# Performance work log

Measured on AMD Instinct MI355X. Metric: run time of the kernel, lower is better.

The kernel has to match this reference:

```python
import jax, jax.numpy as jnp
import numpy as np

N, IN, OUT, E, S = 65536, 512, 512, 8, 64


def setup_inputs() -> dict:
    key = jax.random.key(0)
    k1, k2, k3, k4, k5 = jax.random.split(key, 5)
    bound = float(np.sqrt(1.0 / IN))
    x = jax.random.normal(k1, (N, IN), dtype=jnp.float32)
    expert_coefficients = jax.random.normal(k2, (S, E), dtype=jnp.float32)
    batch_indices = jax.random.randint(k3, (N,), 0, S)
    weights = jax.random.uniform(k4, (E, OUT, IN), dtype=jnp.float32, minval=-bound, maxval=bound)
    bias = jax.random.uniform(k5, (OUT,), dtype=jnp.float32, minval=-bound, maxval=bound)
    return {"x": x, "expert_coefficients": expert_coefficients,
            "batch_indices": batch_indices, "weights": weights, "bias": bias}


def reference(x, expert_coefficients, batch_indices, weights, bias):
    # Original computes mixed_weights[b] = sum_e coeff[b,e] * W[e], then for each
    # system b applies mixed_weights[b] to the atoms with batch_indices == b via a
    # masked scan. Linearity lets us equivalently gather per-atom expert
    # coefficients and contract once, avoiding the O(num_systems * N) waste:
    #   out[n,o] = sum_e coeff[batch_indices[n], e] * sum_i W[e,o,i] * x[n,i]
    coeff_per_atom = expert_coefficients[batch_indices]  # [N, E]
    out = jnp.einsum('ni,eoi,ne->no', x, weights, coeff_per_atom)  # [N, OUT]
    return out + bias
```

## Files before the change

### kernel.cpp

```cpp
#include <hip/hip_runtime.h>
#include <hip/hip_bf16.h>

#define NA   65536
#define DIN  512
#define DOUT 512
#define NE   8
#define NS   64
#define CAP  1280
#define BM   128
#define BN   128
#define BK   32
#define TPS  (CAP / BM)

typedef __attribute__((ext_vector_type(8))) __bf16 bf16x8;
typedef __attribute__((ext_vector_type(4))) float floatx4;

__device__ __forceinline__ void async_load16(const void* g, void* l) {
  __builtin_amdgcn_global_load_lds(
      (__attribute__((address_space(1))) void*)(void*)g,
      (__attribute__((address_space(3))) void*)l,
      16, 0, 0);
}

__global__ void scatter_kernel(const int* __restrict__ bidx,
                               int* __restrict__ counts,
                               int* __restrict__ perm) {
  __shared__ int hist[NS];
  __shared__ int base[NS];
  int t = threadIdx.x;
  if (t < NS) hist[t] = 0;
  __syncthreads();
  int n = blockIdx.x * 256 + t;
  int s = bidx[n];
  int rank = atomicAdd(&hist[s], 1);
  __syncthreads();
  if (t < NS && hist[t] > 0) base[t] = atomicAdd(&counts[t], hist[t]);
  __syncthreads();
  perm[s * CAP + base[s] + rank] = n;
}

__global__ void gather_kernel(const float* __restrict__ x,
                              const int* __restrict__ perm,
                              const int* __restrict__ counts,
                              ushort* __restrict__ xp) {
  int rg = blockIdx.x * 4 + (threadIdx.x >> 6);
  int lane = threadIdx.x & 63;
  int s = rg / CAP;
  int r = rg - s * CAP;
  if (r >= counts[s]) return;
  int pr = perm[rg];
  const float4* src = (const float4*)(x + (size_t)pr * DIN);
  float4 a = src[2 * lane], b = src[2 * lane + 1];
  union { bf16x8 v; uint4 u; } cv;
  cv.v[0] = (__bf16)a.x; cv.v[1] = (__bf16)a.y;
  cv.v[2] = (__bf16)a.z; cv.v[3] = (__bf16)a.w;
  cv.v[4] = (__bf16)b.x; cv.v[5] = (__bf16)b.y;
  cv.v[6] = (__bf16)b.z; cv.v[7] = (__bf16)b.w;
  *(uint4*)(xp + (size_t)rg * DIN + lane * 8) = cv.u;
}

__global__ void mixw_kernel(const float* __restrict__ W,
                            const float* __restrict__ coeff,
                            ushort* __restrict__ mixedW) {
  int t = threadIdx.x;
  int base = blockIdx.x * 2048 + t * 8;
  float w[NE][8];
#pragma unroll
  for (int e = 0; e < NE; e++) {
    const float4* p = (const float4*)(W + e * (DOUT * DIN) + base);
    float4 a = p[0], b = p[1];
    w[e][0] = a.x; w[e][1] = a.y; w[e][2] = a.z; w[e][3] = a.w;
    w[e][4] = b.x; w[e][5] = b.y; w[e][6] = b.z; w[e][7] = b.w;
  }
  int s0 = blockIdx.y * 8;
  for (int si = 0; si < 8; si++) {
    int s = s0 + si;
    float o[8] = {0, 0, 0, 0, 0, 0, 0, 0};
#pragma unroll
    for (int e = 0; e < NE; e++) {
      float c = coeff[s * NE + e];
#pragma unroll
      for (int j = 0; j < 8; j++) o[j] += c * w[e][j];
    }
    union { bf16x8 v; uint4 u; } cv;
#pragma unroll
    for (int j = 0; j < 8; j++) cv.v[j] = (__bf16)o[j];
    *(uint4*)(mixedW + (size_t)s * (DOUT * DIN) + base) = cv.u;
  }
}

__global__ __launch_bounds__(256) void gemm_kernel(
    const ushort* __restrict__ xp, const ushort* __restrict__ mixedW,
    const int* __restrict__ perm, const int* __restrict__ counts,
    const float* __restrict__ bias, float* __restrict__ out) {
  int st = blockIdx.y;
  int s = st / TPS;
  int tt = st - s * TPS;
  int count = counts[s];
  int r0 = tt * BM;
  if (r0 >= count) return;
  int rows = min(BM, count - r0);
  int n0 = blockIdx.x * BN;

  __shared__ __align__(16) ushort Alds[2][BM * BK];
  __shared__ __align__(16) ushort Blds[2][BN * BK];
  __shared__ int prow[BM];

  int tid = threadIdx.x;
  int lane = tid & 63;
  int wave = tid >> 6;

  if (tid < BM) prow[tid] = perm[s * CAP + r0 + min(tid, rows - 1)];

  const ushort* aptr[2];
  const ushort* bptr[2];
  int loff[2];
#pragma unroll
  for (int j = 0; j < 2; j++) {
    int region = j * 4 + wave;
    int row = region * 16 + (lane >> 2);
    int kc = (lane & 3) * 8;
    aptr[j] = xp + (size_t)(s * CAP + r0 + row) * DIN + kc;
    bptr[j] = mixedW + (size_t)s * (DOUT * DIN) + (size_t)(n0 + row) * DIN + kc;
    loff[j] = region * 512;
  }

  floatx4 acc[4][4];
#pragma unroll
  for (int mt = 0; mt < 4; mt++)
#pragma unroll
    for (int nt = 0; nt < 4; nt++) acc[mt][nt] = {0.f, 0.f, 0.f, 0.f};

  int wm = wave >> 1, wn = wave & 1;
  int m15 = lane & 15, quad = lane >> 4;

#pragma unroll
  for (int j = 0; j < 2; j++) {
    async_load16(aptr[j], Alds[0] + loff[j]);
    async_load16(bptr[j], Blds[0] + loff[j]);
  }
  __syncthreads();

  int cur = 0;
  for (int kk = 0; kk < DIN; kk += BK) {
    int nk = kk + BK;
    if (nk < DIN) {
#pragma unroll
      for (int j = 0; j < 2; j++) {
        async_load16(aptr[j] + nk, Alds[cur ^ 1] + loff[j]);
        async_load16(bptr[j] + nk, Blds[cur ^ 1] + loff[j]);
      }
      asm volatile("s_waitcnt vmcnt(4)" ::: "memory");
    } else {
      asm volatile("s_waitcnt vmcnt(0)" ::: "memory");
    }
    __builtin_amdgcn_s_barrier();
    __builtin_amdgcn_sched_barrier(0);

    bf16x8 af[4], bfm[4];
#pragma unroll
    for (int i = 0; i < 4; i++) {
      af[i]  = *(const bf16x8*)(Alds[cur] + (wm * 64 + i * 16 + m15) * BK + quad * 8);
      bfm[i] = *(const bf16x8*)(Blds[cur] + (wn * 64 + i * 16 + m15) * BK + quad * 8);
    }
#pragma unroll
    for (int mt = 0; mt < 4; mt++)
#pragma unroll
      for (int nt = 0; nt < 4; nt++)
        acc[mt][nt] = __builtin_amdgcn_mfma_f32_16x16x32_bf16(
            af[mt], bfm[nt], acc[mt][nt], 0, 0, 0);

    __builtin_amdgcn_sched_barrier(0);
    __builtin_amdgcn_s_barrier();
    cur ^= 1;
  }

  float bv[4];
#pragma unroll
  for (int nt = 0; nt < 4; nt++) bv[nt] = bias[n0 + wn * 64 + nt * 16 + m15];

#pragma unroll
  for (int mt = 0; mt < 4; mt++) {
    int rb = wm * 64 + mt * 16 + quad * 4;
    int pr[4];
#pragma unroll
    for (int r = 0; r < 4; r++) pr[r] = prow[rb + r];
#pragma unroll
    for (int nt = 0; nt < 4; nt++) {
      int col = n0 + wn * 64 + nt * 16 + m15;
#pragma unroll
      for (int r = 0; r < 4; r++) {
        if (rb + r < rows)
          out[(size_t)pr[r] * DOUT + col] = acc[mt][nt][r] + bv[nt];
      }
    }
  }
}

extern "C" void kernel_launch(void* const* d_in, const int* in_sizes, int n_in,
                              void* d_out, int out_size, void* d_ws,
                              size_t ws_size, hipStream_t stream) {
  const float* x     = (const float*)d_in[0];
  const float* coeff = (const float*)d_in[1];
  const int*   bidx  = (const int*)d_in[2];
  const float* W     = (const float*)d_in[3];
  const float* bias  = (const float*)d_in[4];
  float* out = (float*)d_out;

  char* ws = (char*)d_ws;
  int* counts    = (int*)ws;
  int* perm      = (int*)(ws + 1024);
  ushort* mixedW = (ushort*)(ws + 1024 + NS * CAP * 4);
  ushort* xp     = (ushort*)(ws + 1024 + NS * CAP * 4 +
                             (size_t)NS * DOUT * DIN * 2);

  hipMemsetAsync(counts, 0, NS * sizeof(int), stream);
  hipLaunchKernelGGL(scatter_kernel, dim3(NA / 256), dim3(256), 0, stream,
                     bidx, counts, perm);
  hipLaunchKernelGGL(gather_kernel, dim3(NS * CAP / 4), dim3(256), 0, stream,
                     x, perm, counts, xp);
  hipLaunchKernelGGL(mixw_kernel, dim3(DOUT * DIN / 2048, 8), dim3(256), 0,
                     stream, W, coeff, mixedW);
  hipLaunchKernelGGL(gemm_kernel, dim3(DOUT / BN, NS * TPS), dim3(256), 0,
                     stream, xp, mixedW, perm, counts, bias, out);
}
```

Before: 348.6 us.

## Fuse row gather and bf16 conversion into GEMM with triple-buffered fp32 A loads

Removes the separate gather kernel and its bf16 staging copy of x. The GEMM now reads fp32 rows of x through the permutation straight into LDS, converts them to bf16 at fragment-load time, and moves from double to triple buffering. It also remaps workgroups across the 8 XCDs and pads the per-system counters to separate cache lines. In exchange, the A tile takes twice the LDS and global bandwidth, and the conversion adds ALU work inside the main loop. Each x row is also re-read by all four N-tile workgroups instead of once.

Result: slower. 358.0 us (+2.7%).

```diff
diff --git a/kernel.cpp b/kernel.cpp
--- a/kernel.cpp
+++ b/kernel.cpp
@@ -11,6 +11,8 @@
 #define BN   128
 #define BK   32
 #define TPS  (CAP / BM)
+#define NKT  (DIN / BK)
+#define CSTR 32
 
 typedef __attribute__((ext_vector_type(8))) __bf16 bf16x8;
 typedef __attribute__((ext_vector_type(4))) float floatx4;
@@ -34,29 +36,9 @@
   int s = bidx[n];
   int rank = atomicAdd(&hist[s], 1);
   __syncthreads();
-  if (t < NS && hist[t] > 0) base[t] = atomicAdd(&counts[t], hist[t]);
+  if (t < NS && hist[t] > 0) base[t] = atomicAdd(&counts[t * CSTR], hist[t]);
   __syncthreads();
   perm[s * CAP + base[s] + rank] = n;
-}
-
-__global__ void gather_kernel(const float* __restrict__ x,
-                              const int* __restrict__ perm,
-                              const int* __restrict__ counts,
-                              ushort* __restrict__ xp) {
-  int rg = blockIdx.x * 4 + (threadIdx.x >> 6);
-  int lane = threadIdx.x & 63;
-  int s = rg / CAP;
-  int r = rg - s * CAP;
-  if (r >= counts[s]) return;
-  int pr = perm[rg];
-  const float4* src = (const float4*)(x + (size_t)pr * DIN);
-  float4 a = src[2 * lane], b = src[2 * lane + 1];
-  union { bf16x8 v; uint4 u; } cv;
-  cv.v[0] = (__bf16)a.x; cv.v[1] = (__bf16)a.y;
-  cv.v[2] = (__bf16)a.z; cv.v[3] = (__bf16)a.w;
-  cv.v[4] = (__bf16)b.x; cv.v[5] = (__bf16)b.y;
-  cv.v[6] = (__bf16)b.z; cv.v[7] = (__bf16)b.w;
-  *(uint4*)(xp + (size_t)rg * DIN + lane * 8) = cv.u;
 }
 
 __global__ void mixw_kernel(const float* __restrict__ W,
@@ -90,20 +72,26 @@
 }
 
 __global__ __launch_bounds__(256) void gemm_kernel(
-    const ushort* __restrict__ xp, const ushort* __restrict__ mixedW,
+    const float* __restrict__ x, const ushort* __restrict__ mixedW,
     const int* __restrict__ perm, const int* __restrict__ counts,
     const float* __restrict__ bias, float* __restrict__ out) {
-  int st = blockIdx.y;
-  int s = st / TPS;
-  int tt = st - s * TPS;
-  int count = counts[s];
+  int nwg = gridDim.x * gridDim.y;
+  int lin = blockIdx.y * gridDim.x + blockIdx.x;
+  int cpx = nwg >> 3;
+  int work = (lin & 7) * cpx + (lin >> 3);
+  int bx = work & 3;
+  int by = work >> 2;
+
+  int s = by / TPS;
+  int tt = by - s * TPS;
+  int count = counts[s * CSTR];
   int r0 = tt * BM;
   if (r0 >= count) return;
   int rows = min(BM, count - r0);
-  int n0 = blockIdx.x * BN;
-
-  __shared__ __align__(16) ushort Alds[2][BM * BK];
-  __shared__ __align__(16) ushort Blds[2][BN * BK];
+  int n0 = bx * BN;
+
+  __shared__ __align__(16) float  Alds[3][BM * BK];
+  __shared__ __align__(16) ushort Blds[3][BN * BK];
   __shared__ int prow[BM];
 
   int tid = threadIdx.x;
@@ -112,17 +100,25 @@
 
   if (tid < BM) prow[tid] = perm[s * CAP + r0 + min(tid, rows - 1)];
 
-  const ushort* aptr[2];
+  const float* aptr[4];
+  int aoff[4];
+#pragma unroll
+  for (int j = 0; j < 4; j++) {
+    int region = j * 4 + wave;
+    int arow = region * 8 + (lane >> 3);
+    int pr = perm[s * CAP + r0 + min(arow, rows - 1)];
+    aptr[j] = x + (size_t)pr * DIN + (lane & 7) * 4;
+    aoff[j] = region * 256;
+  }
   const ushort* bptr[2];
-  int loff[2];
+  int boff[2];
 #pragma unroll
   for (int j = 0; j < 2; j++) {
     int region = j * 4 + wave;
-    int row = region * 16 + (lane >> 2);
-    int kc = (lane & 3) * 8;
-    aptr[j] = xp + (size_t)(s * CAP + r0 + row) * DIN + kc;
-    bptr[j] = mixedW + (size_t)s * (DOUT * DIN) + (size_t)(n0 + row) * DIN + kc;
-    loff[j] = region * 512;
+    int brow = region * 16 + (lane >> 2);
+    bptr[j] = mixedW + (size_t)s * (DOUT * DIN) + (size_t)(n0 + brow) * DIN +
+              (lane & 3) * 8;
+    boff[j] = region * 512;
   }
 
   floatx4 acc[4][4];
@@ -134,34 +130,49 @@
   int wm = wave >> 1, wn = wave & 1;
   int m15 = lane & 15, quad = lane >> 4;
 
-#pragma unroll
-  for (int j = 0; j < 2; j++) {
-    async_load16(aptr[j], Alds[0] + loff[j]);
-    async_load16(bptr[j], Blds[0] + loff[j]);
-  }
-  __syncthreads();
-
-  int cur = 0;
-  for (int kk = 0; kk < DIN; kk += BK) {
-    int nk = kk + BK;
-    if (nk < DIN) {
-#pragma unroll
-      for (int j = 0; j < 2; j++) {
-        async_load16(aptr[j] + nk, Alds[cur ^ 1] + loff[j]);
-        async_load16(bptr[j] + nk, Blds[cur ^ 1] + loff[j]);
-      }
-      asm volatile("s_waitcnt vmcnt(4)" ::: "memory");
+  __syncthreads();
+
+#pragma unroll
+  for (int t0 = 0; t0 < 2; t0++) {
+#pragma unroll
+    for (int j = 0; j < 4; j++)
+      async_load16(aptr[j] + t0 * BK, Alds[t0] + aoff[j]);
+#pragma unroll
+    for (int j = 0; j < 2; j++)
+      async_load16(bptr[j] + t0 * BK, Blds[t0] + boff[j]);
+  }
+
+  for (int t = 0; t < NKT; ++t) {
+    if (t + 2 < NKT) {
+      int nb = (t + 2) % 3;
+#pragma unroll
+      for (int j = 0; j < 4; j++)
+        async_load16(aptr[j] + (t + 2) * BK, Alds[nb] + aoff[j]);
+#pragma unroll
+      for (int j = 0; j < 2; j++)
+        async_load16(bptr[j] + (t + 2) * BK, Blds[nb] + boff[j]);
+      asm volatile("s_waitcnt vmcnt(12)" ::: "memory");
+    } else if (t == NKT - 2) {
+      asm volatile("s_waitcnt vmcnt(6)" ::: "memory");
     } else {
       asm volatile("s_waitcnt vmcnt(0)" ::: "memory");
     }
     __builtin_amdgcn_s_barrier();
     __builtin_amdgcn_sched_barrier(0);
 
+    int cb = t % 3;
     bf16x8 af[4], bfm[4];
 #pragma unroll
     for (int i = 0; i < 4; i++) {
-      af[i]  = *(const bf16x8*)(Alds[cur] + (wm * 64 + i * 16 + m15) * BK + quad * 8);
-      bfm[i] = *(const bf16x8*)(Blds[cur] + (wn * 64 + i * 16 + m15) * BK + quad * 8);
+      const float* ap = Alds[cb] + (wm * 64 + i * 16 + m15) * BK + quad * 8;
+      floatx4 lo = *(const floatx4*)ap;
+      floatx4 hi = *(const floatx4*)(ap + 4);
+#pragma unroll
+      for (int k = 0; k < 4; k++) {
+        af[i][k] = (__bf16)lo[k];
+        af[i][4 + k] = (__bf16)hi[k];
+      }
+      bfm[i] = *(const bf16x8*)(Blds[cb] + (wn * 64 + i * 16 + m15) * BK + quad * 8);
     }
 #pragma unroll
     for (int mt = 0; mt < 4; mt++)
@@ -172,7 +183,6 @@
 
     __builtin_amdgcn_sched_barrier(0);
     __builtin_amdgcn_s_barrier();
-    cur ^= 1;
   }
 
   float bv[4];
@@ -209,18 +219,14 @@
 
   char* ws = (char*)d_ws;
   int* counts    = (int*)ws;
-  int* perm      = (int*)(ws + 1024);
-  ushort* mixedW = (ushort*)(ws + 1024 + NS * CAP * 4);
-  ushort* xp     = (ushort*)(ws + 1024 + NS * CAP * 4 +
-                             (size_t)NS * DOUT * DIN * 2);
-
-  hipMemsetAsync(counts, 0, NS * sizeof(int), stream);
+  int* perm      = (int*)(ws + NS * CSTR * 4);
+  ushort* mixedW = (ushort*)(ws + NS * CSTR * 4 + NS * CAP * 4);
+
+  hipMemsetAsync(counts, 0, NS * CSTR * sizeof(int), stream);
   hipLaunchKernelGGL(scatter_kernel, dim3(NA / 256), dim3(256), 0, stream,
                      bidx, counts, perm);
-  hipLaunchKernelGGL(gather_kernel, dim3(NS * CAP / 4), dim3(256), 0, stream,
-                     x, perm, counts, xp);
   hipLaunchKernelGGL(mixw_kernel, dim3(DOUT * DIN / 2048, 8), dim3(256), 0,
                      stream, W, coeff, mixedW);
   hipLaunchKernelGGL(gemm_kernel, dim3(DOUT / BN, NS * TPS), dim3(256), 0,
-                     stream, xp, mixedW, perm, counts, bias, out);
-}
+                     stream, x, mixedW, perm, counts, bias, out);
+}
```
